# Kernel tuning notes

Hardware: AMD Instinct MI355X
Metric: run time of the kernel (lower is better)

Reference implementation:

```python
import jax, jax.numpy as jnp
import numpy as np

B, T, V, D, E, H = 32, 64, 32000, 512, 1024, 1024


def setup_inputs() -> dict:
    key = jax.random.key(0)
    ks = jax.random.split(key, 7)
    sc = 0.02
    return {
        "encoder": jax.random.normal(ks[0], (B, E), jnp.float32),
        "gtruths": jax.random.randint(ks[1], (B, T), 0, V),
        "emb": jax.random.normal(ks[2], (V, D), jnp.float32) * sc,
        "W_ih": jax.random.normal(ks[3], (4 * H, E + D), jnp.float32) * sc,
        "W_hh": jax.random.normal(ks[4], (4 * H, H), jnp.float32) * sc,
        "b_ih": jnp.zeros((4 * H,), jnp.float32),
        "b_hh": jnp.zeros((4 * H,), jnp.float32),
        "W_fc": jax.random.normal(ks[5], (V, H), jnp.float32) * sc,
        "b_fc": jnp.zeros((V,), jnp.float32),
        "ssprob": 1,
        "is_train": 1,
    }


def reference(encoder, gtruths, emb, W_ih, W_hh, b_ih, b_hh, W_fc, b_fc, ssprob, is_train):
    # is_train=1, ssprob=1 -> teacher forcing every step (random.random() > 1 is False)
    g = jnp.transpose(emb[gtruths], (1, 0, 2))  # [T, B, D]
    bsz = encoder.shape[0]
    hdim = W_hh.shape[1]

    def step(carry, g_t):
        hx, cx = carry
        inp = jnp.concatenate([encoder, g_t], axis=-1)  # [B, E+D]
        gates = inp @ W_ih.T + b_ih + hx @ W_hh.T + b_hh  # [B, 4H]
        i, f, gg, o = jnp.split(gates, 4, axis=-1)  # torch LSTMCell gate order
        cx_new = jax.nn.sigmoid(f) * cx + jax.nn.sigmoid(i) * jnp.tanh(gg)
        hx_new = jax.nn.sigmoid(o) * jnp.tanh(cx_new)
        logits_t = hx_new @ W_fc.T + b_fc  # [B, V]
        return (hx_new, cx_new), logits_t

    init = (jnp.zeros((bsz, hdim), encoder.dtype), jnp.zeros((bsz, hdim), encoder.dtype))
    _, logits = jax.lax.scan(step, init, g)  # [T, B, V]
    predic = jnp.argmax(logits, axis=-1).T  # [B, T]
    return logits, predic
```

## Files before the change

### kernel.cpp

```cpp
#include <hip/hip_runtime.h>
#include <math.h>

#define B_ 32
#define T_ 64
#define V_ 32000
#define D_ 512
#define E_ 1024
#define H_ 1024
#define G4_ 4096
#define ED_ 1536
#define M_ 2048

typedef unsigned short u16;

using bf16x8 = __attribute__((ext_vector_type(8))) short;
using f32x4  = __attribute__((ext_vector_type(4))) float;

__device__ __forceinline__ u16 f2bf(float x) {
  unsigned u = __float_as_uint(x);
  u += 0x7FFFu + ((u >> 16) & 1u);
  return (u16)(u >> 16);
}
__device__ __forceinline__ float bf2f(u16 h) {
  return __uint_as_float(((unsigned)h) << 16);
}

__global__ __launch_bounds__(256) void build_x(const float* __restrict__ enc,
                                               const int* __restrict__ gt,
                                               const float* __restrict__ emb,
                                               float* __restrict__ X) {
  int m = blockIdx.x;
  int col = blockIdx.y * 256 + threadIdx.x;
  int t = m >> 5, b = m & 31;
  float v;
  if (col < E_) {
    v = enc[b * E_ + col];
  } else {
    int gid = gt[b * T_ + t];
    v = emb[(size_t)gid * D_ + (col - E_)];
  }
  X[(size_t)m * ED_ + col] = v;
}

__global__ __launch_bounds__(256) void bias_sum_k(const float* __restrict__ a,
                                                  const float* __restrict__ b,
                                                  float* __restrict__ o) {
  int i = blockIdx.x * 256 + threadIdx.x;
  if (i < G4_) o[i] = a[i] + b[i];
}

__global__ __launch_bounds__(256) void gemm_abt(const float* __restrict__ A,
                                                const float* __restrict__ Bm,
                                                const float* __restrict__ bias,
                                                float* __restrict__ C,
                                                int M, int N, int K) {
  __shared__ __align__(16) float As[16][128];
  __shared__ __align__(16) float Bs[16][128];
  const int tid = threadIdx.x;
  const int bm = blockIdx.y * 128;
  const int bn = blockIdx.x * 128;
  const int tx = tid & 15, ty = tid >> 4;
  const int lr = tid >> 1;
  const int lk = (tid & 1) * 8;
  const float* Ap = A + (size_t)(bm + lr) * K + lk;
  const float* Bp = Bm + (size_t)(bn + lr) * K + lk;

  float acc[8][8];
#pragma unroll
  for (int i = 0; i < 8; ++i)
#pragma unroll
    for (int j = 0; j < 8; ++j) acc[i][j] = 0.f;

  for (int k0 = 0; k0 < K; k0 += 16) {
    const float4 av0 = *(const float4*)(Ap + k0);
    const float4 av1 = *(const float4*)(Ap + k0 + 4);
    const float4 bv0 = *(const float4*)(Bp + k0);
    const float4 bv1 = *(const float4*)(Bp + k0 + 4);
    __syncthreads();
    As[lk + 0][lr] = av0.x; As[lk + 1][lr] = av0.y;
    As[lk + 2][lr] = av0.z; As[lk + 3][lr] = av0.w;
    As[lk + 4][lr] = av1.x; As[lk + 5][lr] = av1.y;
    As[lk + 6][lr] = av1.z; As[lk + 7][lr] = av1.w;
    Bs[lk + 0][lr] = bv0.x; Bs[lk + 1][lr] = bv0.y;
    Bs[lk + 2][lr] = bv0.z; Bs[lk + 3][lr] = bv0.w;
    Bs[lk + 4][lr] = bv1.x; Bs[lk + 5][lr] = bv1.y;
    Bs[lk + 6][lr] = bv1.z; Bs[lk + 7][lr] = bv1.w;
    __syncthreads();
#pragma unroll
    for (int k = 0; k < 16; ++k) {
      const float4 a0 = *(const float4*)&As[k][ty * 8];
      const float4 a1 = *(const float4*)&As[k][ty * 8 + 4];
      const float4 b0 = *(const float4*)&Bs[k][tx * 8];
      const float4 b1 = *(const float4*)&Bs[k][tx * 8 + 4];
      const float a[8] = {a0.x, a0.y, a0.z, a0.w, a1.x, a1.y, a1.z, a1.w};
      const float b[8] = {b0.x, b0.y, b0.z, b0.w, b1.x, b1.y, b1.z, b1.w};
#pragma unroll
      for (int i = 0; i < 8; ++i)
#pragma unroll
        for (int j = 0; j < 8; ++j)
          acc[i][j] = fmaf(a[i], b[j], acc[i][j]);
    }
  }

#pragma unroll
  for (int i = 0; i < 8; ++i) {
    const int row = bm + ty * 8 + i;
    float* Cp = C + (size_t)row * N + bn + tx * 8;
    float o[8];
#pragma unroll
    for (int j = 0; j < 8; ++j) o[j] = acc[i][j] + bias[bn + tx * 8 + j];
    *(float4*)(Cp)     = make_float4(o[0], o[1], o[2], o[3]);
    *(float4*)(Cp + 4) = make_float4(o[4], o[5], o[6], o[7]);
  }
}

__global__ __launch_bounds__(256) void gemm_bf16x3(
    const u16* __restrict__ Ahi, const u16* __restrict__ Alo,
    const float* __restrict__ Bf, const float* __restrict__ bias,
    float* __restrict__ C, int M, int N, int K) {
  __shared__ __align__(16) u16 Ah_s[128 * 40];
  __shared__ __align__(16) u16 Al_s[128 * 40];
  __shared__ __align__(16) u16 Bh_s[128 * 40];
  __shared__ __align__(16) u16 Bl_s[128 * 40];

  const int tid = threadIdx.x;
  const int bn = blockIdx.x * 128;
  const int bm = blockIdx.y * 128;
  const int wave = tid >> 6, lane = tid & 63;
  const int wm = wave >> 1, wn = wave & 1;
  const int r16 = lane & 15, kj = lane >> 4;

  const int ar = tid >> 1;
  const int ak = (tid & 1) * 16;
  const u16* gAh = Ahi + (size_t)(bm + ar) * K + ak;
  const u16* gAl = Alo + (size_t)(bm + ar) * K + ak;

  const int br = tid >> 3;
  const int bk = (tid & 7) * 4;
  const float* gB = Bf + (size_t)(bn + br) * K + bk;

  f32x4 acc[4][4];
#pragma unroll
  for (int i = 0; i < 4; ++i)
#pragma unroll
    for (int j = 0; j < 4; ++j) acc[i][j] = (f32x4){0.f, 0.f, 0.f, 0.f};

  uint4 pa0 = *(const uint4*)(gAh);
  uint4 pa1 = *(const uint4*)(gAh + 8);
  uint4 pl0 = *(const uint4*)(gAl);
  uint4 pl1 = *(const uint4*)(gAl + 8);
  float4 pb[4];
#pragma unroll
  for (int p = 0; p < 4; ++p) pb[p] = *(const float4*)(gB + (size_t)(p * 32) * K);

  const int abase = (wm * 64 + r16) * 40 + kj * 8;
  const int bbase = (wn * 64 + r16) * 40 + kj * 8;

  for (int k0 = 0; k0 < K; k0 += 32) {
    union { u16 u[4]; uint2 v; } ph[4], pl[4];
#pragma unroll
    for (int p = 0; p < 4; ++p) {
      const float xe[4] = {pb[p].x, pb[p].y, pb[p].z, pb[p].w};
#pragma unroll
      for (int e = 0; e < 4; ++e) {
        const u16 h = f2bf(xe[e]);
        ph[p].u[e] = h;
        pl[p].u[e] = f2bf(xe[e] - bf2f(h));
      }
    }

    __syncthreads();
    *(uint4*)&Ah_s[ar * 40 + ak]     = pa0;
    *(uint4*)&Ah_s[ar * 40 + ak + 8] = pa1;
    *(uint4*)&Al_s[ar * 40 + ak]     = pl0;
    *(uint4*)&Al_s[ar * 40 + ak + 8] = pl1;
#pragma unroll
    for (int p = 0; p < 4; ++p) {
      *(uint2*)&Bh_s[(br + p * 32) * 40 + bk] = ph[p].v;
      *(uint2*)&Bl_s[(br + p * 32) * 40 + bk] = pl[p].v;
    }
    __syncthreads();

    if (k0 + 32 < K) {
      const int kn = k0 + 32;
      pa0 = *(const uint4*)(gAh + kn);
      pa1 = *(const uint4*)(gAh + kn + 8);
      pl0 = *(const uint4*)(gAl + kn);
      pl1 = *(const uint4*)(gAl + kn + 8);
#pragma unroll
      for (int p = 0; p < 4; ++p)
        pb[p] = *(const float4*)(gB + (size_t)(p * 32) * K + kn);
    }

    bf16x8 fah[4], fal[4];
#pragma unroll
    for (int i = 0; i < 4; ++i) {
      fah[i] = *(const bf16x8*)&Ah_s[abase + i * 640];
      fal[i] = *(const bf16x8*)&Al_s[abase + i * 640];
    }
#pragma unroll
    for (int j = 0; j < 4; ++j) {
      const bf16x8 fbh = *(const bf16x8*)&Bh_s[bbase + j * 640];
      const bf16x8 fbl = *(const bf16x8*)&Bl_s[bbase + j * 640];
#pragma unroll
      for (int i = 0; i < 4; ++i) {
        acc[i][j] = __builtin_amdgcn_mfma_f32_16x16x32_bf16(fah[i], fbh, acc[i][j], 0, 0, 0);
        acc[i][j] = __builtin_amdgcn_mfma_f32_16x16x32_bf16(fah[i], fbl, acc[i][j], 0, 0, 0);
        acc[i][j] = __builtin_amdgcn_mfma_f32_16x16x32_bf16(fal[i], fbh, acc[i][j], 0, 0, 0);
      }
    }
  }

#pragma unroll
  for (int j = 0; j < 4; ++j) {
    const int col = bn + wn * 64 + j * 16 + r16;
    const float bv = bias[col];
#pragma unroll
    for (int i = 0; i < 4; ++i) {
      const int row0 = bm + wm * 64 + i * 16 + kj * 4;
#pragma unroll
      for (int q = 0; q < 4; ++q)
        C[(size_t)(row0 + q) * N + col] = acc[i][j][q] + bv;
    }
  }
}

__global__ __launch_bounds__(256) void lstm_gates(const float* __restrict__ hx,
                                                  const float* __restrict__ W_hh,
                                                  float* __restrict__ preact_t) {
  __shared__ __align__(16) float hs[128 * 36];
  const int tid = threadIdx.x;
  const int k0 = blockIdx.x * 128;
  const int h0 = blockIdx.y * 32;

  for (int i = tid; i < 32 * 128; i += 256) {
    int b = i >> 7, k = i & 127;
    hs[k * 36 + b] = hx[b * H_ + k0 + k];
  }
  __syncthreads();

  const int p = tid >> 2;
  const int bo = (tid & 3) * 8;
  const int r0 = p, r1 = p + 64;
  const int j0 = (r0 >> 5) * H_ + h0 + (r0 & 31);
  const int j1 = (r1 >> 5) * H_ + h0 + (r1 & 31);
  const float* w0p = W_hh + (size_t)j0 * H_ + k0;
  const float* w1p = W_hh + (size_t)j1 * H_ + k0;

  float acc0[8], acc1[8];
#pragma unroll
  for (int i = 0; i < 8; ++i) { acc0[i] = 0.f; acc1[i] = 0.f; }

#pragma unroll 4
  for (int kk = 0; kk < 128; kk += 4) {
    const float4 w0 = *(const float4*)(w0p + kk);
    const float4 w1 = *(const float4*)(w1p + kk);
    const float wa[4] = {w0.x, w0.y, w0.z, w0.w};
    const float wb[4] = {w1.x, w1.y, w1.z, w1.w};
#pragma unroll
    for (int i = 0; i < 4; ++i) {
      const float4 h0v = *(const float4*)&hs[(kk + i) * 36 + bo];
      const float4 h1v = *(const float4*)&hs[(kk + i) * 36 + bo + 4];
      acc0[0] = fmaf(wa[i], h0v.x, acc0[0]);
      acc0[1] = fmaf(wa[i], h0v.y, acc0[1]);
      acc0[2] = fmaf(wa[i], h0v.z, acc0[2]);
      acc0[3] = fmaf(wa[i], h0v.w, acc0[3]);
      acc0[4] = fmaf(wa[i], h1v.x, acc0[4]);
      acc0[5] = fmaf(wa[i], h1v.y, acc0[5]);
      acc0[6] = fmaf(wa[i], h1v.z, acc0[6]);
      acc0[7] = fmaf(wa[i], h1v.w, acc0[7]);
      acc1[0] = fmaf(wb[i], h0v.x, acc1[0]);
      acc1[1] = fmaf(wb[i], h0v.y, acc1[1]);
      acc1[2] = fmaf(wb[i], h0v.z, acc1[2]);
      acc1[3] = fmaf(wb[i], h0v.w, acc1[3]);
      acc1[4] = fmaf(wb[i], h1v.x, acc1[4]);
      acc1[5] = fmaf(wb[i], h1v.y, acc1[5]);
      acc1[6] = fmaf(wb[i], h1v.z, acc1[6]);
      acc1[7] = fmaf(wb[i], h1v.w, acc1[7]);
    }
  }

#pragma unroll
  for (int bb = 0; bb < 8; ++bb) {
    atomicAdd(&preact_t[(bo + bb) * G4_ + j0], acc0[bb]);
    atomicAdd(&preact_t[(bo + bb) * G4_ + j1], acc1[bb]);
  }
}

__device__ __forceinline__ float sigf(float x) { return 1.0f / (1.0f + expf(-x)); }

__global__ __launch_bounds__(256) void lstm_cell(const float* __restrict__ pre,
                                                 float* __restrict__ hx,
                                                 float* __restrict__ cx,
                                                 u16* __restrict__ ahi_t,
                                                 u16* __restrict__ alo_t) {
  const int tid = blockIdx.x * 256 + threadIdx.x;
  const int b = tid >> 10, h = tid & 1023;
  const float gi = pre[b * G4_ + h];
  const float gf = pre[b * G4_ + H_ + h];
  const float gg = pre[b * G4_ + 2 * H_ + h];
  const float go = pre[b * G4_ + 3 * H_ + h];
  const float c = cx[tid];
  const float cn = sigf(gf) * c + sigf(gi) * tanhf(gg);
  const float hn = sigf(go) * tanhf(cn);
  cx[tid] = cn;
  hx[tid] = hn;
  const u16 hh = f2bf(hn);
  ahi_t[tid] = hh;
  alo_t[tid] = f2bf(hn - bf2f(hh));
}

__global__ __launch_bounds__(256) void argmax_rows(const float* __restrict__ logits,
                                                   float* __restrict__ predic) {
  const int m = blockIdx.x;
  const float* row = logits + (size_t)m * V_;
  const int tid = threadIdx.x;
  float bv = -3.402823466e38f;
  int bi = V_;
  for (int v = tid; v < V_; v += 256) {
    float x = row[v];
    if (x > bv) { bv = x; bi = v; }
  }
  __shared__ float sv[256];
  __shared__ int si[256];
  sv[tid] = bv; si[tid] = bi;
  __syncthreads();
  for (int s = 128; s > 0; s >>= 1) {
    if (tid < s) {
      if (sv[tid + s] > sv[tid] ||
          (sv[tid + s] == sv[tid] && si[tid + s] < si[tid])) {
        sv[tid] = sv[tid + s];
        si[tid] = si[tid + s];
      }
    }
    __syncthreads();
  }
  if (tid == 0) {
    int t = m >> 5, b = m & 31;
    predic[b * T_ + t] = (float)si[0];
  }
}

extern "C" void kernel_launch(void* const* d_in, const int* in_sizes, int n_in,
                              void* d_out, int out_size, void* d_ws, size_t ws_size,
                              hipStream_t stream) {
  const float* enc  = (const float*)d_in[0];
  const int*   gt   = (const int*)d_in[1];
  const float* emb  = (const float*)d_in[2];
  const float* W_ih = (const float*)d_in[3];
  const float* W_hh = (const float*)d_in[4];
  const float* b_ih = (const float*)d_in[5];
  const float* b_hh = (const float*)d_in[6];
  const float* W_fc = (const float*)d_in[7];
  const float* b_fc = (const float*)d_in[8];

  float* out    = (float*)d_out;
  float* logits = out;
  float* predic = out + (size_t)M_ * V_;

  float* Xbuf   = out;
  float* preact = out + 4194304;

  float* ws     = (float*)d_ws;
  float* hx     = ws;
  float* cx     = ws + 32768;
  float* bsum   = ws + 65536;
  u16* Ahi      = (u16*)(ws + 131072);
  u16* Alo      = Ahi + (size_t)M_ * H_;

  hipMemsetAsync(hx, 0, 32768 * sizeof(float), stream);
  hipMemsetAsync(cx, 0, 32768 * sizeof(float), stream);

  build_x<<<dim3(M_, 6), 256, 0, stream>>>(enc, gt, emb, Xbuf);
  bias_sum_k<<<16, 256, 0, stream>>>(b_ih, b_hh, bsum);

  gemm_abt<<<dim3(G4_ / 128, M_ / 128), 256, 0, stream>>>(
      Xbuf, W_ih, bsum, preact, M_, G4_, ED_);

  for (int t = 0; t < T_; ++t) {
    float* pre_t = preact + (size_t)t * B_ * G4_;
    lstm_gates<<<dim3(8, 32), 256, 0, stream>>>(hx, W_hh, pre_t);
    lstm_cell<<<128, 256, 0, stream>>>(pre_t, hx, cx,
                                       Ahi + (size_t)t * B_ * H_,
                                       Alo + (size_t)t * B_ * H_);
  }

  gemm_bf16x3<<<dim3(V_ / 128, M_ / 128), 256, 0, stream>>>(
      Ahi, Alo, W_fc, b_fc, logits, M_, V_, H_);

  argmax_rows<<<M_, 256, 0, stream>>>(logits, predic);
}
```

Measured before the change: 2.170 ms.

## Fuse LSTM recurrence into persistent cooperative kernel with MFMA and split-bf16 input GEMM

Replaces the 128 per-timestep gate and cell kernel launches with a single cooperative persistent kernel. Each block keeps its slice of W_hh in LDS as split bf16, computes the recurrent product with MFMA, applies the cell update with the cell state held in registers, and uses grid.sync between steps. The input projection GEMM moves from FP32 SIMT to the bf16x3 MFMA kernel and writes a transposed layout for coalesced per-step reads. The design depends on all 256 blocks being co-resident, and the bf16x3 split may change numerics slightly.

Result: slower. 4.618 ms (+112.8%).

```diff
diff --git a/kernel.cpp b/kernel.cpp
--- a/kernel.cpp
+++ b/kernel.cpp
@@ -1,5 +1,8 @@
 #include <hip/hip_runtime.h>
+#include <hip/hip_cooperative_groups.h>
 #include <math.h>
+
+namespace cg = cooperative_groups;
 
 #define B_ 32
 #define T_ 64
@@ -24,11 +27,13 @@
 __device__ __forceinline__ float bf2f(u16 h) {
   return __uint_as_float(((unsigned)h) << 16);
 }
-
-__global__ __launch_bounds__(256) void build_x(const float* __restrict__ enc,
-                                               const int* __restrict__ gt,
-                                               const float* __restrict__ emb,
-                                               float* __restrict__ X) {
+__device__ __forceinline__ float sigf(float x) { return 1.0f / (1.0f + expf(-x)); }
+
+__global__ __launch_bounds__(256) void build_x_split(const float* __restrict__ enc,
+                                                     const int* __restrict__ gt,
+                                                     const float* __restrict__ emb,
+                                                     u16* __restrict__ Xhi,
+                                                     u16* __restrict__ Xlo) {
   int m = blockIdx.x;
   int col = blockIdx.y * 256 + threadIdx.x;
   int t = m >> 5, b = m & 31;
@@ -39,7 +44,9 @@
     int gid = gt[b * T_ + t];
     v = emb[(size_t)gid * D_ + (col - E_)];
   }
-  X[(size_t)m * ED_ + col] = v;
+  const u16 h = f2bf(v);
+  Xhi[(size_t)m * ED_ + col] = h;
+  Xlo[(size_t)m * ED_ + col] = f2bf(v - bf2f(h));
 }
 
 __global__ __launch_bounds__(256) void bias_sum_k(const float* __restrict__ a,
@@ -49,71 +56,7 @@
   if (i < G4_) o[i] = a[i] + b[i];
 }
 
-__global__ __launch_bounds__(256) void gemm_abt(const float* __restrict__ A,
-                                                const float* __restrict__ Bm,
-                                                const float* __restrict__ bias,
-                                                float* __restrict__ C,
-                                                int M, int N, int K) {
-  __shared__ __align__(16) float As[16][128];
-  __shared__ __align__(16) float Bs[16][128];
-  const int tid = threadIdx.x;
-  const int bm = blockIdx.y * 128;
-  const int bn = blockIdx.x * 128;
-  const int tx = tid & 15, ty = tid >> 4;
-  const int lr = tid >> 1;
-  const int lk = (tid & 1) * 8;
-  const float* Ap = A + (size_t)(bm + lr) * K + lk;
-  const float* Bp = Bm + (size_t)(bn + lr) * K + lk;
-
-  float acc[8][8];
-#pragma unroll
-  for (int i = 0; i < 8; ++i)
-#pragma unroll
-    for (int j = 0; j < 8; ++j) acc[i][j] = 0.f;
-
-  for (int k0 = 0; k0 < K; k0 += 16) {
-    const float4 av0 = *(const float4*)(Ap + k0);
-    const float4 av1 = *(const float4*)(Ap + k0 + 4);
-    const float4 bv0 = *(const float4*)(Bp + k0);
-    const float4 bv1 = *(const float4*)(Bp + k0 + 4);
-    __syncthreads();
-    As[lk + 0][lr] = av0.x; As[lk + 1][lr] = av0.y;
-    As[lk + 2][lr] = av0.z; As[lk + 3][lr] = av0.w;
-    As[lk + 4][lr] = av1.x; As[lk + 5][lr] = av1.y;
-    As[lk + 6][lr] = av1.z; As[lk + 7][lr] = av1.w;
-    Bs[lk + 0][lr] = bv0.x; Bs[lk + 1][lr] = bv0.y;
-    Bs[lk + 2][lr] = bv0.z; Bs[lk + 3][lr] = bv0.w;
-    Bs[lk + 4][lr] = bv1.x; Bs[lk + 5][lr] = bv1.y;
-    Bs[lk + 6][lr] = bv1.z; Bs[lk + 7][lr] = bv1.w;
-    __syncthreads();
-#pragma unroll
-    for (int k = 0; k < 16; ++k) {
-      const float4 a0 = *(const float4*)&As[k][ty * 8];
-      const float4 a1 = *(const float4*)&As[k][ty * 8 + 4];
-      const float4 b0 = *(const float4*)&Bs[k][tx * 8];
-      const float4 b1 = *(const float4*)&Bs[k][tx * 8 + 4];
-      const float a[8] = {a0.x, a0.y, a0.z, a0.w, a1.x, a1.y, a1.z, a1.w};
-      const float b[8] = {b0.x, b0.y, b0.z, b0.w, b1.x, b1.y, b1.z, b1.w};
-#pragma unroll
-      for (int i = 0; i < 8; ++i)
-#pragma unroll
-        for (int j = 0; j < 8; ++j)
-          acc[i][j] = fmaf(a[i], b[j], acc[i][j]);
-    }
-  }
-
-#pragma unroll
-  for (int i = 0; i < 8; ++i) {
-    const int row = bm + ty * 8 + i;
-    float* Cp = C + (size_t)row * N + bn + tx * 8;
-    float o[8];
-#pragma unroll
-    for (int j = 0; j < 8; ++j) o[j] = acc[i][j] + bias[bn + tx * 8 + j];
-    *(float4*)(Cp)     = make_float4(o[0], o[1], o[2], o[3]);
-    *(float4*)(Cp + 4) = make_float4(o[4], o[5], o[6], o[7]);
-  }
-}
-
+template <int TRANS_OUT>
 __global__ __launch_bounds__(256) void gemm_bf16x3(
     const u16* __restrict__ Ahi, const u16* __restrict__ Alo,
     const float* __restrict__ Bf, const float* __restrict__ bias,
@@ -218,96 +161,116 @@
 #pragma unroll
     for (int i = 0; i < 4; ++i) {
       const int row0 = bm + wm * 64 + i * 16 + kj * 4;
-#pragma unroll
-      for (int q = 0; q < 4; ++q)
-        C[(size_t)(row0 + q) * N + col] = acc[i][j][q] + bv;
-    }
-  }
-}
-
-__global__ __launch_bounds__(256) void lstm_gates(const float* __restrict__ hx,
-                                                  const float* __restrict__ W_hh,
-                                                  float* __restrict__ preact_t) {
-  __shared__ __align__(16) float hs[128 * 36];
+      if (TRANS_OUT) {
+        float* p = C + ((size_t)(row0 >> 5) * G4_ + col) * B_ + (row0 & 31);
+        *(float4*)p = make_float4(acc[i][j][0] + bv, acc[i][j][1] + bv,
+                                  acc[i][j][2] + bv, acc[i][j][3] + bv);
+      } else {
+#pragma unroll
+        for (int q = 0; q < 4; ++q)
+          C[(size_t)(row0 + q) * N + col] = acc[i][j][q] + bv;
+      }
+    }
+  }
+}
+
+__global__ __launch_bounds__(256) void lstm_loop(const float* __restrict__ W_hh,
+                                                 const float* __restrict__ preT,
+                                                 u16* __restrict__ Ahi,
+                                                 u16* __restrict__ Alo) {
+  cg::grid_group grid = cg::this_grid();
+  const int g = blockIdx.x;
   const int tid = threadIdx.x;
-  const int k0 = blockIdx.x * 128;
-  const int h0 = blockIdx.y * 32;
-
-  for (int i = tid; i < 32 * 128; i += 256) {
-    int b = i >> 7, k = i & 127;
-    hs[k * 36 + b] = hx[b * H_ + k0 + k];
-  }
+  const int wave = tid >> 6, lane = tid & 63;
+  const int r16 = lane & 15, kj = lane >> 4;
+
+  __shared__ __align__(16) u16 Wh[16][1032];
+  __shared__ __align__(16) u16 Wl[16][1032];
+  __shared__ __align__(16) float red[4][2][64][4];
+  __shared__ float pre_s[16][32];
+  __shared__ float gsm[32][17];
+
+  for (int idx = tid; idx < 16 * 1024; idx += 256) {
+    const int r = idx >> 10, k = idx & 1023;
+    const int j = (r >> 2) * H_ + 4 * g + (r & 3);
+    const float w = W_hh[(size_t)j * H_ + k];
+    const u16 h = f2bf(w);
+    Wh[r][k] = h;
+    Wl[r][k] = f2bf(w - bf2f(h));
+  }
+  float creg[4] = {0.f, 0.f, 0.f, 0.f};
   __syncthreads();
 
-  const int p = tid >> 2;
-  const int bo = (tid & 3) * 8;
-  const int r0 = p, r1 = p + 64;
-  const int j0 = (r0 >> 5) * H_ + h0 + (r0 & 31);
-  const int j1 = (r1 >> 5) * H_ + h0 + (r1 & 31);
-  const float* w0p = W_hh + (size_t)j0 * H_ + k0;
-  const float* w1p = W_hh + (size_t)j1 * H_ + k0;
-
-  float acc0[8], acc1[8];
-#pragma unroll
-  for (int i = 0; i < 8; ++i) { acc0[i] = 0.f; acc1[i] = 0.f; }
-
-#pragma unroll 4
-  for (int kk = 0; kk < 128; kk += 4) {
-    const float4 w0 = *(const float4*)(w0p + kk);
-    const float4 w1 = *(const float4*)(w1p + kk);
-    const float wa[4] = {w0.x, w0.y, w0.z, w0.w};
-    const float wb[4] = {w1.x, w1.y, w1.z, w1.w};
-#pragma unroll
-    for (int i = 0; i < 4; ++i) {
-      const float4 h0v = *(const float4*)&hs[(kk + i) * 36 + bo];
-      const float4 h1v = *(const float4*)&hs[(kk + i) * 36 + bo + 4];
-      acc0[0] = fmaf(wa[i], h0v.x, acc0[0]);
-      acc0[1] = fmaf(wa[i], h0v.y, acc0[1]);
-      acc0[2] = fmaf(wa[i], h0v.z, acc0[2]);
-      acc0[3] = fmaf(wa[i], h0v.w, acc0[3]);
-      acc0[4] = fmaf(wa[i], h1v.x, acc0[4]);
-      acc0[5] = fmaf(wa[i], h1v.y, acc0[5]);
-      acc0[6] = fmaf(wa[i], h1v.z, acc0[6]);
-      acc0[7] = fmaf(wa[i], h1v.w, acc0[7]);
-      acc1[0] = fmaf(wb[i], h0v.x, acc1[0]);
-      acc1[1] = fmaf(wb[i], h0v.y, acc1[1]);
-      acc1[2] = fmaf(wb[i], h0v.z, acc1[2]);
-      acc1[3] = fmaf(wb[i], h0v.w, acc1[3]);
-      acc1[4] = fmaf(wb[i], h1v.x, acc1[4]);
-      acc1[5] = fmaf(wb[i], h1v.y, acc1[5]);
-      acc1[6] = fmaf(wb[i], h1v.z, acc1[6]);
-      acc1[7] = fmaf(wb[i], h1v.w, acc1[7]);
-    }
-  }
-
-#pragma unroll
-  for (int bb = 0; bb < 8; ++bb) {
-    atomicAdd(&preact_t[(bo + bb) * G4_ + j0], acc0[bb]);
-    atomicAdd(&preact_t[(bo + bb) * G4_ + j1], acc1[bb]);
-  }
-}
-
-__device__ __forceinline__ float sigf(float x) { return 1.0f / (1.0f + expf(-x)); }
-
-__global__ __launch_bounds__(256) void lstm_cell(const float* __restrict__ pre,
-                                                 float* __restrict__ hx,
-                                                 float* __restrict__ cx,
-                                                 u16* __restrict__ ahi_t,
-                                                 u16* __restrict__ alo_t) {
-  const int tid = blockIdx.x * 256 + threadIdx.x;
-  const int b = tid >> 10, h = tid & 1023;
-  const float gi = pre[b * G4_ + h];
-  const float gf = pre[b * G4_ + H_ + h];
-  const float gg = pre[b * G4_ + 2 * H_ + h];
-  const float go = pre[b * G4_ + 3 * H_ + h];
-  const float c = cx[tid];
-  const float cn = sigf(gf) * c + sigf(gi) * tanhf(gg);
-  const float hn = sigf(go) * tanhf(cn);
-  cx[tid] = cn;
-  hx[tid] = hn;
-  const u16 hh = f2bf(hn);
-  ahi_t[tid] = hh;
-  alo_t[tid] = f2bf(hn - bf2f(hh));
+  for (int t = 0; t < T_; ++t) {
+    const int i1 = tid + 256;
+    const int r0 = tid >> 5, b0 = tid & 31;
+    const int r1 = i1 >> 5, b1 = i1 & 31;
+    const float pv0 = preT[((size_t)t * G4_ + (r0 >> 2) * H_ + 4 * g + (r0 & 3)) * B_ + b0];
+    const float pv1 = preT[((size_t)t * G4_ + (r1 >> 2) * H_ + 4 * g + (r1 & 3)) * B_ + b1];
+
+    f32x4 acc[2];
+    acc[0] = (f32x4){0.f, 0.f, 0.f, 0.f};
+    acc[1] = (f32x4){0.f, 0.f, 0.f, 0.f};
+    if (t > 0) {
+      const u16* Ah = Ahi + (size_t)(t - 1) * B_ * H_;
+      const u16* Al = Alo + (size_t)(t - 1) * B_ * H_;
+      const int kbase = wave * 256;
+#pragma unroll
+      for (int kt = 0; kt < 8; ++kt) {
+        const int k = kbase + kt * 32 + kj * 8;
+        const bf16x8 bh = *(const bf16x8*)&Wh[r16][k];
+        const bf16x8 bl = *(const bf16x8*)&Wl[r16][k];
+#pragma unroll
+        for (int mi = 0; mi < 2; ++mi) {
+          const bf16x8 ah = *(const bf16x8*)(Ah + (size_t)(mi * 16 + r16) * H_ + k);
+          const bf16x8 al = *(const bf16x8*)(Al + (size_t)(mi * 16 + r16) * H_ + k);
+          acc[mi] = __builtin_amdgcn_mfma_f32_16x16x32_bf16(ah, bh, acc[mi], 0, 0, 0);
+          acc[mi] = __builtin_amdgcn_mfma_f32_16x16x32_bf16(ah, bl, acc[mi], 0, 0, 0);
+          acc[mi] = __builtin_amdgcn_mfma_f32_16x16x32_bf16(al, bh, acc[mi], 0, 0, 0);
+        }
+      }
+    }
+
+    __syncthreads();
+    *(f32x4*)&red[wave][0][lane][0] = acc[0];
+    *(f32x4*)&red[wave][1][lane][0] = acc[1];
+    pre_s[r0][b0] = pv0;
+    pre_s[r1][b1] = pv1;
+    __syncthreads();
+
+    for (int o = tid; o < 512; o += 256) {
+      const int mi = o >> 8, l = (o >> 2) & 63, q = o & 3;
+      const float s = red[0][mi][l][q] + red[1][mi][l][q] +
+                      red[2][mi][l][q] + red[3][mi][l][q];
+      const int b = mi * 16 + (l >> 4) * 4 + q;
+      const int r = l & 15;
+      gsm[b][r] = s + pre_s[r][b];
+    }
+    __syncthreads();
+
+    if (tid < 32) {
+      const int b = tid;
+      ushort4 hh, hl;
+      u16* hhp = &hh.x; u16* hlp = &hl.x;
+#pragma unroll
+      for (int il = 0; il < 4; ++il) {
+        const float gi = gsm[b][il];
+        const float gf = gsm[b][4 + il];
+        const float gg = gsm[b][8 + il];
+        const float go = gsm[b][12 + il];
+        const float cn = sigf(gf) * creg[il] + sigf(gi) * tanhf(gg);
+        const float hn = sigf(go) * tanhf(cn);
+        creg[il] = cn;
+        const u16 h16 = f2bf(hn);
+        hhp[il] = h16;
+        hlp[il] = f2bf(hn - bf2f(h16));
+      }
+      *(ushort4*)&Ahi[(size_t)(t * B_ + b) * H_ + 4 * g] = hh;
+      *(ushort4*)&Alo[(size_t)(t * B_ + b) * H_ + 4 * g] = hl;
+    }
+    __threadfence();
+    grid.sync();
+  }
 }
 
 __global__ __launch_bounds__(256) void argmax_rows(const float* __restrict__ logits,
@@ -358,34 +321,28 @@
   float* logits = out;
   float* predic = out + (size_t)M_ * V_;
 
-  float* Xbuf   = out;
-  float* preact = out + 4194304;
+  u16*   Xhi    = (u16*)out;
+  u16*   Xlo    = Xhi + (size_t)M_ * ED_;
+  float* preT   = out + 4194304;
 
   float* ws     = (float*)d_ws;
-  float* hx     = ws;
-  float* cx     = ws + 32768;
-  float* bsum   = ws + 65536;
-  u16* Ahi      = (u16*)(ws + 131072);
-  u16* Alo      = Ahi + (size_t)M_ * H_;
-
-  hipMemsetAsync(hx, 0, 32768 * sizeof(float), stream);
-  hipMemsetAsync(cx, 0, 32768 * sizeof(float), stream);
-
-  build_x<<<dim3(M_, 6), 256, 0, stream>>>(enc, gt, emb, Xbuf);
+  float* bsum   = ws;
+  u16*   Ahi    = (u16*)(ws + 4096);
+  u16*   Alo    = Ahi + (size_t)M_ * H_;
+
+  build_x_split<<<dim3(M_, 6), 256, 0, stream>>>(enc, gt, emb, Xhi, Xlo);
   bias_sum_k<<<16, 256, 0, stream>>>(b_ih, b_hh, bsum);
 
-  gemm_abt<<<dim3(G4_ / 128, M_ / 128), 256, 0, stream>>>(
-      Xbuf, W_ih, bsum, preact, M_, G4_, ED_);
-
-  for (int t = 0; t < T_; ++t) {
-    float* pre_t = preact + (size_t)t * B_ * G4_;
-    lstm_gates<<<dim3(8, 32), 256, 0, stream>>>(hx, W_hh, pre_t);
-    lstm_cell<<<128, 256, 0, stream>>>(pre_t, hx, cx,
-                                       Ahi + (size_t)t * B_ * H_,
-                                       Alo + (size_t)t * B_ * H_);
-  }
-
-  gemm_bf16x3<<<dim3(V_ / 128, M_ / 128), 256, 0, stream>>>(
+  gemm_bf16x3<1><<<dim3(G4_ / 128, M_ / 128), 256, 0, stream>>>(
+      Xhi, Xlo, W_ih, bsum, preT, M_, G4_, ED_);
+
+  {
+    void* args[] = {(void*)&W_hh, (void*)&preT, (void*)&Ahi, (void*)&Alo};
+    hipLaunchCooperativeKernel((void*)lstm_loop, dim3(256), dim3(256), args, 0,
+                               stream);
+  }
+
+  gemm_bf16x3<0><<<dim3(V_ / 128, M_ / 128), 256, 0, stream>>>(
       Ahi, Alo, W_fc, b_fc, logits, M_, V_, H_);
 
   argmax_rows<<<M_, 256, 0, stream>>>(logits, predic);
```
